# Kernel optimization log

Hardware: AMD Instinct MI355X
Metric: run time of the kernel (lower is better)

## Reference

```python
import jax, jax.numpy as jnp
import numpy as np

N_M, N_D, E, D, H, O = 50000, 20000, 600000, 128, 128, 64


def _graph_conv(x_src, x_dst, src, dst, W_rel, b_rel, W_root, ew=None):
    # PyG GraphConv: lin_rel(scatter_add(msg)) + lin_root(x_dst)
    msg = x_src[src]                       # [E, d_src] gather
    if ew is not None:
        msg = msg * ew[:, None]            # edge-weighted messages
    agg = jax.ops.segment_sum(msg, dst, num_segments=x_dst.shape[0])  # [N_dst, d_src]
    return agg @ W_rel + b_rel + x_dst @ W_root


def setup_inputs() -> dict:
    key = jax.random.key(0)
    ks = jax.random.split(key, 16)
    s = 1.0 / np.sqrt(D)
    inp = {
        "x_meas": jax.random.normal(ks[0], (N_M, D), jnp.float32),
        "x_dem": jax.random.normal(ks[1], (N_D, D), jnp.float32),
        "src_m": jax.random.randint(ks[2], (E,), 0, N_M, jnp.int32),
        "dst_m": jax.random.randint(ks[3], (E,), 0, N_M, jnp.int32),
        "src_b": jax.random.randint(ks[4], (E,), 0, N_M, jnp.int32),
        "dst_b": jax.random.randint(ks[5], (E,), 0, N_D, jnp.int32),
        "edge_weight": jax.random.normal(ks[6], (E,), jnp.float32),
        "W_rel1": jax.random.normal(ks[7], (D, H), jnp.float32) * s,
        "b_rel1": jnp.zeros((H,), jnp.float32),
        "W_root1": jax.random.normal(ks[8], (D, H), jnp.float32) * s,
        "W_rel2": jax.random.normal(ks[9], (D, H), jnp.float32) * s,
        "b_rel2": jnp.zeros((H,), jnp.float32),
        "W_root2": jax.random.normal(ks[10], (D, H), jnp.float32) * s,
        "W_rel3": jax.random.normal(ks[11], (H, H), jnp.float32) * s,
        "b_rel3": jnp.zeros((H,), jnp.float32),
        "W_root3": jax.random.normal(ks[12], (H, H), jnp.float32) * s,
        "W_lin": jax.random.normal(ks[13], (H, O), jnp.float32) * (1.0 / np.sqrt(H)),
        "b_lin": jnp.zeros((O,), jnp.float32),
    }
    return inp


def reference(x_meas, x_dem, src_m, dst_m, src_b, dst_b, edge_weight,
              W_rel1, b_rel1, W_root1, W_rel2, b_rel2, W_root2,
              W_rel3, b_rel3, W_root3, W_lin, b_lin):
    ew = jax.nn.sigmoid(edge_weight)
    movie_x = jax.nn.relu(_graph_conv(x_meas, x_meas, src_m, dst_m, W_rel1, b_rel1, W_root1))
    user_x = jax.nn.relu(_graph_conv(x_meas, x_dem, src_b, dst_b, W_rel2, b_rel2, W_root2, ew))
    user_x = jax.nn.relu(_graph_conv(movie_x, user_x, src_b, dst_b, W_rel3, b_rel3, W_root3, ew))
    return user_x @ W_lin + b_lin  # [N_D, O]
```

## Files before the change

kernel.cpp:

```cpp
#include <hip/hip_runtime.h>


typedef unsigned short u16;
typedef unsigned int u32;
typedef __attribute__((ext_vector_type(8))) short bf16x8;
typedef __attribute__((ext_vector_type(4))) float f32x4;

#define NMC 50000
#define NDC 20000
#define EC  600000
#define CM  128
#define CHM ((EC + CM - 1) / CM)
#define NWM8 (NMC / 4)
#define NWD8 (NDC / 4)

__device__ __forceinline__ float bf2f(u16 h) {
    union { u32 u; float f; } v; v.u = ((u32)h) << 16; return v.f;
}
__device__ __forceinline__ float uplo(u32 u) {
    union { u32 u; float f; } t; t.u = u << 16; return t.f;
}
__device__ __forceinline__ float uphi(u32 u) {
    union { u32 u; float f; } t; t.u = u & 0xffff0000u; return t.f;
}
__device__ __forceinline__ u16 f2bf(float f) {
    union { float f; u32 u; } v; v.f = f;
    u32 lsb = (v.u >> 16) & 1u;
    v.u += 0x7fffu + lsb;
    return (u16)(v.u >> 16);
}

__global__ __launch_bounds__(256)
void prep_hist(const int* __restrict__ dst_m, const int* __restrict__ dst_b,
               int* __restrict__ rank_m, int* __restrict__ rank_b,
               u32* __restrict__ histm, u32* __restrict__ histd,
               const float* __restrict__ xm, u16* __restrict__ xm_bf, int n8m,
               const float* __restrict__ xd, u16* __restrict__ xd_bf, int n8d,
               const float* __restrict__ w0, const float* __restrict__ w1,
               const float* __restrict__ w2, const float* __restrict__ w3,
               const float* __restrict__ w4, const float* __restrict__ w5,
               const float* __restrict__ w6, u16* __restrict__ wbuf,
               int TB, int TB2)
{
    __shared__ u32 h[NWM8];
    const int b = blockIdx.x;
    if (b < 2 * CM) {
        const bool isM = b < CM;
        const int nw = isM ? NWM8 : NWD8;
        for (int i = threadIdx.x; i < nw; i += 256) h[i] = 0;
        __syncthreads();
        if (isM) {
            const int e0 = b * CHM;
            const int e1 = min(EC, e0 + CHM);
            for (int e = e0 + threadIdx.x; e < e1; e += 256) {
                int d = dst_m[e];
                int sh = (d & 3) * 8;
                u32 old = atomicAdd(&h[d >> 2], 1u << sh);
                rank_m[e] = (old >> sh) & 0xffu;
            }
            __syncthreads();
            for (int i = threadIdx.x; i < nw; i += 256)
                histm[(size_t)b * NWM8 + i] = h[i];
        } else {
            const int bb = b - CM;
            const int e0 = bb * CHM;
            const int e1 = min(EC, e0 + CHM);
            for (int e = e0 + threadIdx.x; e < e1; e += 256) {
                int d = dst_b[e];
                int sh = (d & 3) * 8;
                u32 old = atomicAdd(&h[d >> 2], 1u << sh);
                rank_b[e] = (old >> sh) & 0xffu;
            }
            __syncthreads();
            for (int i = threadIdx.x; i < nw; i += 256)
                histd[(size_t)bb * NWD8 + i] = h[i];
        }
        return;
    }
    const int pb = b - 2 * CM;
    if (pb < TB + TB2) {
        const bool isM = pb < TB;
        const float* src = isM ? xm : xd;
        u16* dst = isM ? xm_bf : xd_bf;
        int n8 = isM ? n8m : n8d;
        int i = (pb - (isM ? 0 : TB)) * 256 + threadIdx.x;
        if (i >= n8) return;
        float4 a = ((const float4*)src)[2 * i];
        float4 c2 = ((const float4*)src)[2 * i + 1];
        ushort4 h0; h0.x = f2bf(a.x); h0.y = f2bf(a.y); h0.z = f2bf(a.z); h0.w = f2bf(a.w);
        ushort4 h1; h1.x = f2bf(c2.x); h1.y = f2bf(c2.y); h1.z = f2bf(c2.z); h1.w = f2bf(c2.w);
        ((ushort4*)dst)[2 * i]     = h0;
        ((ushort4*)dst)[2 * i + 1] = h1;
    } else {
        int bb = pb - TB - TB2;
        const int widx = bb >> 6;
        const int o    = ((bb & 63) << 8) + threadIdx.x;
        const int OC   = (widx == 6) ? 64 : 128;
        if (o >= OC * 128) return;
        const float* W;
        switch (widx) {
            case 0: W = w0; break; case 1: W = w1; break; case 2: W = w2; break;
            case 3: W = w3; break; case 4: W = w4; break; case 5: W = w5; break;
            default: W = w6;
        }
        int j = o & 7;
        int lane = (o >> 3) & 63;
        int n, c;
        if (OC == 128) { n = (o >> 9) & 7; c = o >> 12; }
        else           { n = (o >> 9) & 3; c = o >> 11; }
        int col = n * 16 + (lane & 15);
        int k   = c * 32 + (lane >> 4) * 8 + j;
        wbuf[widx * 16384 + o] = f2bf(W[k * OC + col]);
    }
}

__global__ __launch_bounds__(256)
void basescan8(u32* __restrict__ histm, u32* __restrict__ histd,
               int* __restrict__ deg_m, int* __restrict__ deg_b)
{
    int t = blockIdx.x * 256 + threadIdx.x;
    int idx = t >> 2;
    const int q = t & 3;
    u32* hist; int* deg; int NW;
    if (idx < NWM8)             { hist = histm; deg = deg_m; NW = NWM8; }
    else if (idx < NWM8 + NWD8) { hist = histd; deg = deg_b; NW = NWD8; idx -= NWM8; }
    else return;

    u32* hp = hist + (size_t)(q * 32) * NW + idx;
    u32 v[32];
#pragma unroll
    for (int j = 0; j < 32; ++j) v[j] = hp[(size_t)j * NW];
    u32 run = 0;
#pragma unroll
    for (int j = 0; j < 32; ++j) { u32 x = v[j]; v[j] = run; run += x; }
    u32 x = run;
    u32 y = __shfl_up(x, 1, 4); if (q >= 1) x += y;
    y = __shfl_up(x, 2, 4);     if (q >= 2) x += y;
    const u32 base = x - run;
#pragma unroll
    for (int j = 0; j < 32; ++j) hp[(size_t)j * NW] = base + v[j];
    if (q == 3) {
        deg[4 * idx + 0] = (int)(x & 0xffu);
        deg[4 * idx + 1] = (int)((x >> 8) & 0xffu);
        deg[4 * idx + 2] = (int)((x >> 16) & 0xffu);
        deg[4 * idx + 3] = (int)(x >> 24);
    }
}

__device__ __forceinline__ int wave_incl_scan(int v, int lane) {
#pragma unroll
    for (int off = 1; off < 64; off <<= 1) {
        int t = __shfl_up(v, off, 64);
        if (lane >= off) v += t;
    }
    return v;
}

__global__ __launch_bounds__(1024)
void scan2_kernel(const int* __restrict__ degA, int* __restrict__ rpA, int nA,
                  const int* __restrict__ degB, int* __restrict__ rpB, int nB)
{
    const int* deg = blockIdx.x ? degB : degA;
    int* rp = blockIdx.x ? rpB : rpA;
    int n = blockIdx.x ? nB : nA;

    __shared__ int wsum[16];
    __shared__ int carry;
    const int tid = threadIdx.x, lane = tid & 63, wid = tid >> 6;
    if (tid == 0) carry = 0;
    __syncthreads();

    for (int base = 0; base < n; base += 8192) {
        int idx = base + tid * 8;
        int4 va = make_int4(0, 0, 0, 0), vb = make_int4(0, 0, 0, 0);
        if (idx + 7 < n) {
            va = *(const int4*)(deg + idx);
            vb = *(const int4*)(deg + idx + 4);
        } else {
            if (idx + 0 < n) va.x = deg[idx + 0];
            if (idx + 1 < n) va.y = deg[idx + 1];
            if (idx + 2 < n) va.z = deg[idx + 2];
            if (idx + 3 < n) va.w = deg[idx + 3];
            if (idx + 4 < n) vb.x = deg[idx + 4];
            if (idx + 5 < n) vb.y = deg[idx + 5];
            if (idx + 6 < n) vb.z = deg[idx + 6];
            if (idx + 7 < n) vb.w = deg[idx + 7];
        }
        int sa = va.x + va.y + va.z + va.w;
        int s = sa + vb.x + vb.y + vb.z + vb.w;
        int incl = wave_incl_scan(s, lane);
        if (lane == 63) wsum[wid] = incl;
        __syncthreads();
        if (wid == 0) {
            int t = (lane < 16) ? wsum[lane] : 0;
            int ti = wave_incl_scan(t, lane);
            if (lane < 16) wsum[lane] = ti - t;
        }
        __syncthreads();
        int base_t = carry + wsum[wid] + incl - s;
        if (idx + 7 < n) {
            int4 st;
            st.x = base_t;
            st.y = base_t + va.x;
            st.z = base_t + va.x + va.y;
            st.w = base_t + va.x + va.y + va.z;
            *(int4*)(rp + idx) = st;
            int b4 = base_t + sa;
            st.x = b4;
            st.y = b4 + vb.x;
            st.z = b4 + vb.x + vb.y;
            st.w = b4 + vb.x + vb.y + vb.z;
            *(int4*)(rp + idx + 4) = st;
        } else {
            int r = base_t;
            if (idx + 0 < n) rp[idx + 0] = r; r += va.x;
            if (idx + 1 < n) rp[idx + 1] = r; r += va.y;
            if (idx + 2 < n) rp[idx + 2] = r; r += va.z;
            if (idx + 3 < n) rp[idx + 3] = r; r += va.w;
            if (idx + 4 < n) rp[idx + 4] = r; r += vb.x;
            if (idx + 5 < n) rp[idx + 5] = r; r += vb.y;
            if (idx + 6 < n) rp[idx + 6] = r; r += vb.z;
            if (idx + 7 < n) rp[idx + 7] = r;
        }
        __syncthreads();
        if (tid == 1023) carry += wsum[15] + incl;
        __syncthreads();
    }
    if (tid == 0) rp[n] = carry;
}

__global__ __launch_bounds__(256)
void fill_kernel(const int* __restrict__ src_m, const int* __restrict__ dst_m,
                 const int* __restrict__ src_b, const int* __restrict__ dst_b,
                 const float* __restrict__ edge_w,
                 const int* __restrict__ rp_m, const int* __restrict__ rp_b,
                 const int* __restrict__ rank_m, const int* __restrict__ rank_b,
                 const u32* __restrict__ histm, const u32* __restrict__ histd,
                 int* __restrict__ srcs_m, int2* __restrict__ edges_b, int E)
{
    int t = blockIdx.x * 256 + threadIdx.x;
    if (t < E) {
        int d = dst_m[t];
        int c = t / CHM;
        u32 pk = histm[(size_t)c * NWM8 + (d >> 2)];
        int base = (pk >> ((d & 3) * 8)) & 0xffu;
        int pos = rp_m[d] + base + rank_m[t];
        srcs_m[pos] = src_m[t];
    } else if (t < 2 * E) {
        int e = t - E;
        int d = dst_b[e];
        int c = e / CHM;
        u32 pkb = histd[(size_t)c * NWD8 + (d >> 2)];
        int base = (pkb >> ((d & 3) * 8)) & 0xffu;
        int pos = rp_b[d] + base + rank_b[e];
        float x = edge_w[e];
        int2 pk;
        pk.x = src_b[e];
        pk.y = __float_as_int(1.0f / (1.0f + __expf(-x)));
        edges_b[pos] = pk;
    }
}

__global__ __launch_bounds__(256)
void gather12(const u16* __restrict__ Xb,
              const int* __restrict__ srcs_m, const int2* __restrict__ edges_b,
              const int* __restrict__ rp_m, const int* __restrict__ rp_b,
              u16* __restrict__ agg1, u16* __restrict__ agg2, int NM, int ND)
{
    const int h  = blockIdx.x * 16 + (threadIdx.x >> 4);
    const int cl = threadIdx.x & 15;
    float a0 = 0.f, a1 = 0.f, a2 = 0.f, a3 = 0.f;
    float a4 = 0.f, a5 = 0.f, a6 = 0.f, a7 = 0.f;

    if (h < NM) {
        int i   = rp_m[h];
        int end = rp_m[h + 1];
        for (; i + 8 <= end; i += 8) {
            int s[8];
#pragma unroll
            for (int k = 0; k < 8; ++k) s[k] = srcs_m[i + k];
            uint4 v[8];
#pragma unroll
            for (int k = 0; k < 8; ++k)
                v[k] = *(const uint4*)(Xb + (size_t)s[k] * 128 + cl * 8);
#pragma unroll
            for (int k = 0; k < 8; ++k) {
                a0 += uplo(v[k].x); a1 += uphi(v[k].x);
                a2 += uplo(v[k].y); a3 += uphi(v[k].y);
                a4 += uplo(v[k].z); a5 += uphi(v[k].z);
                a6 += uplo(v[k].w); a7 += uphi(v[k].w);
            }
        }
        for (; i < end; ++i) {
            uint4 v = *(const uint4*)(Xb + (size_t)srcs_m[i] * 128 + cl * 8);
            a0 += uplo(v.x); a1 += uphi(v.x);
            a2 += uplo(v.y); a3 += uphi(v.y);
            a4 += uplo(v.z); a5 += uphi(v.z);
            a6 += uplo(v.w); a7 += uphi(v.w);
        }
        uint4 st;
        st.x = (u32)f2bf(a0) | ((u32)f2bf(a1) << 16);
        st.y = (u32)f2bf(a2) | ((u32)f2bf(a3) << 16);
        st.z = (u32)f2bf(a4) | ((u32)f2bf(a5) << 16);
        st.w = (u32)f2bf(a6) | ((u32)f2bf(a7) << 16);
        *(uint4*)(agg1 + (size_t)h * 128 + cl * 8) = st;
    } else if (h < NM + ND) {
        int node = h - NM;
        int i   = rp_b[node];
        int end = rp_b[node + 1];
        for (; i + 8 <= end; i += 8) {
            int2 p[8];
#pragma unroll
            for (int k = 0; k < 8; ++k) p[k] = edges_b[i + k];
            uint4 v[8];
#pragma unroll
            for (int k = 0; k < 8; ++k)
                v[k] = *(const uint4*)(Xb + (size_t)p[k].x * 128 + cl * 8);
#pragma unroll
            for (int k = 0; k < 8; ++k) {
                float w = __int_as_float(p[k].y);
                a0 = fmaf(w, uplo(v[k].x), a0); a1 = fmaf(w, uphi(v[k].x), a1);
                a2 = fmaf(w, uplo(v[k].y), a2); a3 = fmaf(w, uphi(v[k].y), a3);
                a4 = fmaf(w, uplo(v[k].z), a4); a5 = fmaf(w, uphi(v[k].z), a5);
                a6 = fmaf(w, uplo(v[k].w), a6); a7 = fmaf(w, uphi(v[k].w), a7);
            }
        }
        for (; i < end; ++i) {
            int2 pk = edges_b[i];
            float w = __int_as_float(pk.y);
            uint4 v = *(const uint4*)(Xb + (size_t)pk.x * 128 + cl * 8);
            a0 = fmaf(w, uplo(v.x), a0); a1 = fmaf(w, uphi(v.x), a1);
            a2 = fmaf(w, uplo(v.y), a2); a3 = fmaf(w, uphi(v.y), a3);
            a4 = fmaf(w, uplo(v.z), a4); a5 = fmaf(w, uphi(v.z), a5);
            a6 = fmaf(w, uplo(v.w), a6); a7 = fmaf(w, uphi(v.w), a7);
        }
        uint4 st;
        st.x = (u32)f2bf(a0) | ((u32)f2bf(a1) << 16);
        st.y = (u32)f2bf(a2) | ((u32)f2bf(a3) << 16);
        st.z = (u32)f2bf(a4) | ((u32)f2bf(a5) << 16);
        st.w = (u32)f2bf(a6) | ((u32)f2bf(a7) << 16);
        *(uint4*)(agg2 + (size_t)node * 128 + cl * 8) = st;
    }
}

__global__ __launch_bounds__(256)
void gather3_kernel(const u16* __restrict__ Mv, const int2* __restrict__ edges_b,
                    const int* __restrict__ rp_b, u16* __restrict__ agg3, int ND)
{
    const int node = blockIdx.x * 16 + (threadIdx.x >> 4);
    if (node >= ND) return;
    const int cl = threadIdx.x & 15;
    int i   = rp_b[node];
    int end = rp_b[node + 1];
    float a0 = 0.f, a1 = 0.f, a2 = 0.f, a3 = 0.f;
    float a4 = 0.f, a5 = 0.f, a6 = 0.f, a7 = 0.f;

    for (; i + 8 <= end; i += 8) {
        int2 p[8];
#pragma unroll
        for (int k = 0; k < 8; ++k) p[k] = edges_b[i + k];
        uint4 v[8];
#pragma unroll
        for (int k = 0; k < 8; ++k)
            v[k] = *(const uint4*)(Mv + (size_t)p[k].x * 128 + cl * 8);
#pragma unroll
        for (int k = 0; k < 8; ++k) {
            float w = __int_as_float(p[k].y);
            a0 = fmaf(w, uplo(v[k].x), a0); a1 = fmaf(w, uphi(v[k].x), a1);
            a2 = fmaf(w, uplo(v[k].y), a2); a3 = fmaf(w, uphi(v[k].y), a3);
            a4 = fmaf(w, uplo(v[k].z), a4); a5 = fmaf(w, uphi(v[k].z), a5);
            a6 = fmaf(w, uplo(v[k].w), a6); a7 = fmaf(w, uphi(v[k].w), a7);
        }
    }
    for (; i < end; ++i) {
        int2 pk = edges_b[i];
        float w = __int_as_float(pk.y);
        uint4 v = *(const uint4*)(Mv + (size_t)pk.x * 128 + cl * 8);
        a0 = fmaf(w, uplo(v.x), a0); a1 = fmaf(w, uphi(v.x), a1);
        a2 = fmaf(w, uplo(v.y), a2); a3 = fmaf(w, uphi(v.y), a3);
        a4 = fmaf(w, uplo(v.z), a4); a5 = fmaf(w, uphi(v.z), a5);
        a6 = fmaf(w, uplo(v.w), a6); a7 = fmaf(w, uphi(v.w), a7);
    }
    uint4 st;
    st.x = (u32)f2bf(a0) | ((u32)f2bf(a1) << 16);
    st.y = (u32)f2bf(a2) | ((u32)f2bf(a3) << 16);
    st.z = (u32)f2bf(a4) | ((u32)f2bf(a5) << 16);
    st.w = (u32)f2bf(a6) | ((u32)f2bf(a7) << 16);
    *(uint4*)(agg3 + (size_t)node * 128 + cl * 8) = st;
}

__global__ __launch_bounds__(256)
void conv12_mfma(const u16* __restrict__ agg1, const u16* __restrict__ w1r,
                 const float* __restrict__ b1, const u16* __restrict__ xm_bf,
                 const u16* __restrict__ w1o, u16* __restrict__ C1, int N1, int cb1,
                 const u16* __restrict__ agg2, const u16* __restrict__ w2r,
                 const float* __restrict__ b2, const u16* __restrict__ xd_bf,
                 const u16* __restrict__ w2o, u16* __restrict__ C2, int N2)
{
    __shared__ u16 sW[16384];

    const bool seg1 = (int)blockIdx.x < cb1;
    const u16 *A0, *A1p, *Wr, *Wo; const float* bias; u16* C; int N, base;
    if (seg1) { A0 = agg1; A1p = xm_bf; Wr = w1r; Wo = w1o; bias = b1; C = C1; N = N1; base = blockIdx.x; }
    else      { A0 = agg2; A1p = xd_bf; Wr = w2r; Wo = w2o; bias = b2; C = C2; N = N2; base = blockIdx.x - cb1; }

    const int tid  = threadIdx.x;
    const int lane = tid & 63;
    const int m0   = (base * 4 + (tid >> 6)) * 32;
    const int lr   = lane & 15;
    const int quad = lane >> 4;

    int r0 = m0 + lr;      if (r0 >= N) r0 = N - 1;
    int r1 = m0 + 16 + lr; if (r1 >= N) r1 = N - 1;

    f32x4 acc[2][8];
#pragma unroll
    for (int mt = 0; mt < 2; ++mt)
#pragma unroll
        for (int n = 0; n < 8; ++n) acc[mt][n] = (f32x4){0.f, 0.f, 0.f, 0.f};

    for (int i = tid; i < 2048; i += 256)
        ((uint4*)sW)[i] = ((const uint4*)Wr)[i];
    __syncthreads();
#pragma unroll
    for (int c = 0; c < 4; ++c) {
        const int kb = c * 32 + quad * 8;
        bf16x8 a0 = *(const bf16x8*)(A0 + (size_t)r0 * 128 + kb);
        bf16x8 a1 = *(const bf16x8*)(A0 + (size_t)r1 * 128 + kb);
        const u16* wp = sW + c * 4096 + lane * 8;
#pragma unroll
        for (int n = 0; n < 8; ++n) {
            bf16x8 b = *(const bf16x8*)(wp + n * 512);
            acc[0][n] = __builtin_amdgcn_mfma_f32_16x16x32_bf16(a0, b, acc[0][n], 0, 0, 0);
            acc[1][n] = __builtin_amdgcn_mfma_f32_16x16x32_bf16(a1, b, acc[1][n], 0, 0, 0);
        }
    }
    __syncthreads();

    for (int i = tid; i < 2048; i += 256)
        ((uint4*)sW)[i] = ((const uint4*)Wo)[i];
    __syncthreads();
#pragma unroll
    for (int c = 0; c < 4; ++c) {
        const int kb = c * 32 + quad * 8;
        bf16x8 a0 = *(const bf16x8*)(A1p + (size_t)r0 * 128 + kb);
        bf16x8 a1 = *(const bf16x8*)(A1p + (size_t)r1 * 128 + kb);
        const u16* wp = sW + c * 4096 + lane * 8;
#pragma unroll
        for (int n = 0; n < 8; ++n) {
            bf16x8 b = *(const bf16x8*)(wp + n * 512);
            acc[0][n] = __builtin_amdgcn_mfma_f32_16x16x32_bf16(a0, b, acc[0][n], 0, 0, 0);
            acc[1][n] = __builtin_amdgcn_mfma_f32_16x16x32_bf16(a1, b, acc[1][n], 0, 0, 0);
        }
    }

#pragma unroll
    for (int mt = 0; mt < 2; ++mt) {
#pragma unroll
        for (int n = 0; n < 8; ++n) {
            const int col = n * 16 + lr;
            const float b = bias[col];
#pragma unroll
            for (int r = 0; r < 4; ++r) {
                int row = m0 + mt * 16 + quad * 4 + r;
                if (row >= N) continue;
                C[(size_t)row * 128 + col] = f2bf(fmaxf(acc[mt][n][r] + b, 0.f));
            }
        }
    }
}

__global__ __launch_bounds__(256)
void conv3_lin(const u16* __restrict__ A1, const u16* __restrict__ Wr,
               const float* __restrict__ bias3,
               const u16* __restrict__ A2, const u16* __restrict__ Wo,
               const u16* __restrict__ Wl, const float* __restrict__ bias_l,
               float* __restrict__ out, int N)
{
    __shared__ u16 lds[17408 + 8192];
    u16* tile = lds;
    u16* sWl  = lds + 17408;

    const int tid  = threadIdx.x;
    const int lane = tid & 63;
    const int wv   = tid >> 6;
    const int wbase = wv * 32;
    const int m0   = (blockIdx.x * 4 + wv) * 32;
    const int lr   = lane & 15;
    const int quad = lane >> 4;

    int r0 = m0 + lr;      if (r0 >= N) r0 = N - 1;
    int r1 = m0 + 16 + lr; if (r1 >= N) r1 = N - 1;

    f32x4 acc[2][8];
#pragma unroll
    for (int mt = 0; mt < 2; ++mt)
#pragma unroll
        for (int n = 0; n < 8; ++n) acc[mt][n] = (f32x4){0.f, 0.f, 0.f, 0.f};

    for (int i = tid; i < 1024; i += 256)
        ((uint4*)sWl)[i] = ((const uint4*)Wl)[i];
    for (int i = tid; i < 2048; i += 256)
        ((uint4*)lds)[i] = ((const uint4*)Wr)[i];
    __syncthreads();
#pragma unroll
    for (int c = 0; c < 4; ++c) {
        const int kb = c * 32 + quad * 8;
        bf16x8 a0 = *(const bf16x8*)(A1 + (size_t)r0 * 128 + kb);
        bf16x8 a1 = *(const bf16x8*)(A1 + (size_t)r1 * 128 + kb);
        const u16* wp = lds + c * 4096 + lane * 8;
#pragma unroll
        for (int n = 0; n < 8; ++n) {
            bf16x8 b = *(const bf16x8*)(wp + n * 512);
            acc[0][n] = __builtin_amdgcn_mfma_f32_16x16x32_bf16(a0, b, acc[0][n], 0, 0, 0);
            acc[1][n] = __builtin_amdgcn_mfma_f32_16x16x32_bf16(a1, b, acc[1][n], 0, 0, 0);
        }
    }
    __syncthreads();
    for (int i = tid; i < 2048; i += 256)
        ((uint4*)lds)[i] = ((const uint4*)Wo)[i];
    __syncthreads();
// ... 36 lines not shown
#pragma unroll
    for (int c = 0; c < 4; ++c) {
        const int kb = c * 32 + quad * 8;
        bf16x8 a0 = *(const bf16x8*)(tile + (wbase + lr) * 136 + kb);
        bf16x8 a1 = *(const bf16x8*)(tile + (wbase + 16 + lr) * 136 + kb);
#pragma unroll
        for (int n = 0; n < 4; ++n) {
            bf16x8 b = *(const bf16x8*)(sWl + c * 2048 + n * 512 + lane * 8);
            acc2[0][n] = __builtin_amdgcn_mfma_f32_16x16x32_bf16(a0, b, acc2[0][n], 0, 0, 0);
            acc2[1][n] = __builtin_amdgcn_mfma_f32_16x16x32_bf16(a1, b, acc2[1][n], 0, 0, 0);
        }
    }

#pragma unroll
    for (int mt = 0; mt < 2; ++mt) {
#pragma unroll
        for (int n = 0; n < 4; ++n) {
            const int col = n * 16 + lr;
            const float b = bias_l[col];
#pragma unroll
            for (int r = 0; r < 4; ++r) {
                int row = m0 + mt * 16 + quad * 4 + r;
                if (row >= N) continue;
                out[(size_t)row * 64 + col] = acc2[mt][n][r] + b;
            }
        }
    }
}

extern "C" void kernel_launch(void* const* d_in, const int* in_sizes, int n_in,
                              void* d_out, int out_size, void* d_ws, size_t ws_size,
                              hipStream_t stream)
{
    const float* x_meas  = (const float*)d_in[0];
    const float* x_dem   = (const float*)d_in[1];
    const int*   src_m   = (const int*)d_in[2];
    const int*   dst_m   = (const int*)d_in[3];
    const int*   src_b   = (const int*)d_in[4];
    const int*   dst_b   = (const int*)d_in[5];
    const float* edge_w  = (const float*)d_in[6];
    const float* W_rel1  = (const float*)d_in[7];
    const float* b_rel1  = (const float*)d_in[8];
    const float* W_root1 = (const float*)d_in[9];
    const float* W_rel2  = (const float*)d_in[10];
    const float* b_rel2  = (const float*)d_in[11];
    const float* W_root2 = (const float*)d_in[12];
    const float* W_rel3  = (const float*)d_in[13];
    const float* b_rel3  = (const float*)d_in[14];
    const float* W_root3 = (const float*)d_in[15];
    const float* W_lin   = (const float*)d_in[16];
    const float* b_lin   = (const float*)d_in[17];
    float* out = (float*)d_out;

    const int NM = NMC, ND = NDC, E = EC;

    char* p = (char*)d_ws;
    auto alloc = [&](size_t bytes) { char* r = p; p += (bytes + 511) & ~(size_t)511; return r; };
    u32*   histm   = (u32*)alloc((size_t)CM * NWM8 * 4);
    u32*   histd   = (u32*)alloc((size_t)CM * NWD8 * 4);
    int*   deg_m   = (int*)alloc((size_t)NM * 4);
    int*   deg_b   = (int*)alloc((size_t)ND * 4);
    int*   rp_m    = (int*)alloc((size_t)(NM + 1) * 4);
    int*   rp_b    = (int*)alloc((size_t)(ND + 1) * 4);
    int*   srcs_m  = (int*)alloc((size_t)E * 4);
    int2*  edges_b = (int2*)alloc((size_t)E * 8);
    u16*   agg1    = (u16*)alloc((size_t)NM * 128 * 2);
    u16*   agg2    = (u16*)alloc((size_t)ND * 128 * 2);
    u16*   movie   = (u16*)alloc((size_t)NM * 128 * 2);
    u16*   t2      = (u16*)alloc((size_t)ND * 128 * 2);
    u16*   xd_bf   = (u16*)alloc((size_t)ND * 128 * 2);
    u16*   wbuf    = (u16*)alloc(7 * 16384 * 2);
    int* rank_m = (int*)agg1;
    int* rank_b = rank_m + E;
    u16* xm_bf  = movie;
    u16* agg3   = agg1;

    const int TB  = (NM * 16 + 255) / 256;
    const int TB2 = (ND * 16 + 255) / 256;
    const int WB  = 448;
    const int HB  = (2 * E + 255) / 256;

    prep_hist<<<2 * CM + TB + TB2 + WB, 256, 0, stream>>>(
        dst_m, dst_b, rank_m, rank_b, histm, histd,
        x_meas, xm_bf, NM * 16, x_dem, xd_bf, ND * 16,
        W_rel1, W_root1, W_rel2, W_root2, W_rel3, W_root3, W_lin, wbuf,
        TB, TB2);

    basescan8<<<((NWM8 + NWD8) * 4 + 255) / 256, 256, 0, stream>>>(histm, histd, deg_m, deg_b);
    scan2_kernel<<<2, 1024, 0, stream>>>(deg_m, rp_m, NM, deg_b, rp_b, ND);
    fill_kernel<<<HB, 256, 0, stream>>>(src_m, dst_m, src_b, dst_b, edge_w,
                                        rp_m, rp_b, rank_m, rank_b,
                                        histm, histd, srcs_m, edges_b, E);

    gather12<<<(NM + ND + 15) / 16, 256, 0, stream>>>(xm_bf, srcs_m, edges_b,
                                                      rp_m, rp_b, agg1, agg2, NM, ND);

    const int cb1 = (NM + 127) / 128;
    const int cb2 = (ND + 127) / 128;
    u16* w1r = wbuf + 0 * 16384; u16* w1o = wbuf + 1 * 16384;
    u16* w2r = wbuf + 2 * 16384; u16* w2o = wbuf + 3 * 16384;
    u16* w3r = wbuf + 4 * 16384; u16* w3o = wbuf + 5 * 16384;
    u16* wl  = wbuf + 6 * 16384;
    conv12_mfma<<<cb1 + cb2, 256, 0, stream>>>(agg1, w1r, b_rel1, xm_bf, w1o, movie, NM, cb1,
                                               agg2, w2r, b_rel2, xd_bf, w2o, t2,    ND);

    gather3_kernel<<<(ND + 15) / 16, 256, 0, stream>>>(movie, edges_b, rp_b, agg3, ND);

    conv3_lin<<<cb2, 256, 0, stream>>>(agg3, w3r, b_rel3, t2, w3o, wl, b_lin, out, ND);
}
```

Baseline: 269.9 us.

## Fuse scan, fill, gather and conv stages into one flag-synchronized persistent kernel

Replaces the separate basescan, scan, fill, gather, conv12 and gather3 launches with a single kernel. Block ranges act as stages and wait on global atomic counters set by earlier stages, which removes several kernel launch boundaries and lets later stages start as soon as their inputs are posted. The device-wide scan is also reworked to use 256 threads with 32 elements each. xm_bf gets its own buffer instead of aliasing movie, and the flags are zeroed by an extra prep_hist block. This depends on blocks being dispatched in index order to avoid deadlock, and it adds spin-wait overhead, including a whole-grid barrier before the gather stage.

```diff
diff --git a/kernel.cpp b/kernel.cpp
--- a/kernel.cpp
+++ b/kernel.cpp
@@ -14,6 +14,22 @@
 #define NWM8 (NMC / 4)
 #define NWD8 (NDC / 4)
 
+#define B_P0 274
+#define O1 274
+#define O2 276
+#define O3 4964
+#define O4 9339
+#define O5 9887
+#define PEND 11137
+#define CB1 391
+#define CB2 157
+
+#define F_BASE 0
+#define F_SCAN 1
+#define F_FILL 2
+#define F_CONV1 3
+#define F_CFLAG 8
+
 __device__ __forceinline__ float bf2f(u16 h) {
     union { u32 u; float f; } v; v.u = ((u32)h) << 16; return v.f;
 }
@@ -28,6 +44,34 @@
     u32 lsb = (v.u >> 16) & 1u;
     v.u += 0x7fffu + lsb;
     return (u16)(v.u >> 16);
+}
+
+__device__ __forceinline__ void wait_flag(int* flag, int thresh) {
+    if (threadIdx.x == 0) {
+        int it = 0;
+        while (__hip_atomic_load(flag, __ATOMIC_RELAXED, __HIP_MEMORY_SCOPE_AGENT) < thresh) {
+            __builtin_amdgcn_s_sleep(2);
+            if (++it > 100000000) break;
+        }
+        __builtin_amdgcn_fence(__ATOMIC_ACQUIRE, "agent");
+    }
+    __syncthreads();
+}
+__device__ __forceinline__ void post_flag(int* flag, int inc) {
+    __syncthreads();
+    if (threadIdx.x == 0) {
+        __builtin_amdgcn_fence(__ATOMIC_RELEASE, "agent");
+        __hip_atomic_fetch_add(flag, inc, __ATOMIC_RELAXED, __HIP_MEMORY_SCOPE_AGENT);
+    }
+}
+
+__device__ __forceinline__ int wave_incl_scan(int v, int lane) {
+#pragma unroll
+    for (int off = 1; off < 64; off <<= 1) {
+        int t = __shfl_up(v, off, 64);
+        if (lane >= off) v += t;
+    }
+    return v;
 }
 
 __global__ __launch_bounds__(256)
@@ -40,7 +84,7 @@
                const float* __restrict__ w2, const float* __restrict__ w3,
                const float* __restrict__ w4, const float* __restrict__ w5,
                const float* __restrict__ w6, u16* __restrict__ wbuf,
-               int TB, int TB2)
+               int* __restrict__ flags, int TB, int TB2)
 {
     __shared__ u32 h[NWM8];
     const int b = blockIdx.x;
@@ -93,6 +137,10 @@
         ((ushort4*)dst)[2 * i + 1] = h1;
     } else {
         int bb = pb - TB - TB2;
+        if (bb >= 448) {
+            for (int i = threadIdx.x; i < 1024; i += 256) flags[i] = 0;
+            return;
+        }
         const int widx = bb >> 6;
         const int o    = ((bb & 63) << 8) + threadIdx.x;
         const int OC   = (widx == 6) ? 64 : 128;
@@ -115,199 +163,277 @@
 }
 
 __global__ __launch_bounds__(256)
-void basescan8(u32* __restrict__ histm, u32* __restrict__ histd,
-               int* __restrict__ deg_m, int* __restrict__ deg_b)
+void pipeline(u32* __restrict__ histm, u32* __restrict__ histd,
+              int* __restrict__ deg_m, int* __restrict__ deg_b,
+              int* __restrict__ rp_m, int* __restrict__ rp_b,
+              const int* __restrict__ src_m, const int* __restrict__ dst_m,
+              const int* __restrict__ src_b, const int* __restrict__ dst_b,
+              const float* __restrict__ edge_w,
+              const int* __restrict__ rank_m, const int* __restrict__ rank_b,
+              int* __restrict__ srcs_m, int2* __restrict__ edges_b,
+              const u16* __restrict__ xm_bf, const u16* __restrict__ xd_bf,
+              u16* __restrict__ agg1, u16* __restrict__ agg2,
+              const u16* __restrict__ wbuf,
+              const float* __restrict__ b1, const float* __restrict__ b2,
+              u16* __restrict__ movie, u16* __restrict__ t2,
+              u16* __restrict__ agg3, int* __restrict__ flags)
 {
-    int t = blockIdx.x * 256 + threadIdx.x;
-    int idx = t >> 2;
-    const int q = t & 3;
-    u32* hist; int* deg; int NW;
-    if (idx < NWM8)             { hist = histm; deg = deg_m; NW = NWM8; }
-    else if (idx < NWM8 + NWD8) { hist = histd; deg = deg_b; NW = NWD8; idx -= NWM8; }
-    else return;
-
-    u32* hp = hist + (size_t)(q * 32) * NW + idx;
-    u32 v[32];
-#pragma unroll
-    for (int j = 0; j < 32; ++j) v[j] = hp[(size_t)j * NW];
-    u32 run = 0;
-#pragma unroll
-    for (int j = 0; j < 32; ++j) { u32 x = v[j]; v[j] = run; run += x; }
-    u32 x = run;
-    u32 y = __shfl_up(x, 1, 4); if (q >= 1) x += y;
-    y = __shfl_up(x, 2, 4);     if (q >= 2) x += y;
-    const u32 base = x - run;
-#pragma unroll
-    for (int j = 0; j < 32; ++j) hp[(size_t)j * NW] = base + v[j];
-    if (q == 3) {
-        deg[4 * idx + 0] = (int)(x & 0xffu);
-        deg[4 * idx + 1] = (int)((x >> 8) & 0xffu);
-        deg[4 * idx + 2] = (int)((x >> 16) & 0xffu);
-        deg[4 * idx + 3] = (int)(x >> 24);
-    }
-}
-
-__device__ __forceinline__ int wave_incl_scan(int v, int lane) {
-#pragma unroll
-    for (int off = 1; off < 64; off <<= 1) {
-        int t = __shfl_up(v, off, 64);
-        if (lane >= off) v += t;
-    }
-    return v;
-}
-
-__global__ __launch_bounds__(1024)
-void scan2_kernel(const int* __restrict__ degA, int* __restrict__ rpA, int nA,
-                  const int* __restrict__ degB, int* __restrict__ rpB, int nB)
-{
-    const int* deg = blockIdx.x ? degB : degA;
-    int* rp = blockIdx.x ? rpB : rpA;
-    int n = blockIdx.x ? nB : nA;
-
-    __shared__ int wsum[16];
-    __shared__ int carry;
-    const int tid = threadIdx.x, lane = tid & 63, wid = tid >> 6;
-    if (tid == 0) carry = 0;
-    __syncthreads();
-
-    for (int base = 0; base < n; base += 8192) {
-        int idx = base + tid * 8;
-        int4 va = make_int4(0, 0, 0, 0), vb = make_int4(0, 0, 0, 0);
-        if (idx + 7 < n) {
-            va = *(const int4*)(deg + idx);
-            vb = *(const int4*)(deg + idx + 4);
+    const int b   = blockIdx.x;
+    const int tid = threadIdx.x;
+
+    if (b < B_P0) {
+        int t = b * 256 + tid;
+        int idx = t >> 2;
+        const int q = t & 3;
+        u32* hist; int* deg; int NW;
+        bool act = true;
+        if (idx < NWM8)             { hist = histm; deg = deg_m; NW = NWM8; }
+        else if (idx < NWM8 + NWD8) { hist = histd; deg = deg_b; NW = NWD8; idx -= NWM8; }
+        else act = false;
+        if (act) {
+            u32* hp = hist + (size_t)(q * 32) * NW + idx;
+            u32 v[32];
+#pragma unroll
+            for (int j = 0; j < 32; ++j) v[j] = hp[(size_t)j * NW];
+            u32 run = 0;
+#pragma unroll
+            for (int j = 0; j < 32; ++j) { u32 x = v[j]; v[j] = run; run += x; }
+            u32 x = run;
+            u32 y = __shfl_up(x, 1, 4); if (q >= 1) x += y;
+            y = __shfl_up(x, 2, 4);     if (q >= 2) x += y;
+            const u32 base = x - run;
+#pragma unroll
+            for (int j = 0; j < 32; ++j) hp[(size_t)j * NW] = base + v[j];
+            if (q == 3) {
+                deg[4 * idx + 0] = (int)(x & 0xffu);
+                deg[4 * idx + 1] = (int)((x >> 8) & 0xffu);
+                deg[4 * idx + 2] = (int)((x >> 16) & 0xffu);
+                deg[4 * idx + 3] = (int)(x >> 24);
+            }
+        }
+        post_flag(&flags[F_BASE], 1);
+    } else if (b < O2) {
+        wait_flag(&flags[F_BASE], B_P0);
+        const bool isM = (b == O1);
+        const int* deg = isM ? deg_m : deg_b;
+        int* rp = isM ? rp_m : rp_b;
+        const int n = isM ? NMC : NDC;
+        __shared__ int ws4[4], wx4[4];
+        __shared__ int carryS;
+        if (tid == 0) carryS = 0;
+        __syncthreads();
+        const int lane = tid & 63, wid = tid >> 6;
+        for (int base = 0; base < n; base += 8192) {
+            int idx = base + tid * 32;
+            int v[32];
+#pragma unroll
+            for (int k = 0; k < 8; ++k) {
+                int4 qv = make_int4(0, 0, 0, 0);
+                int i4 = idx + 4 * k;
+                if (i4 + 3 < n) qv = *(const int4*)(deg + i4);
+                else {
+                    if (i4 + 0 < n) qv.x = deg[i4 + 0];
+                    if (i4 + 1 < n) qv.y = deg[i4 + 1];
+                    if (i4 + 2 < n) qv.z = deg[i4 + 2];
+                    if (i4 + 3 < n) qv.w = deg[i4 + 3];
+                }
+                v[4 * k] = qv.x; v[4 * k + 1] = qv.y; v[4 * k + 2] = qv.z; v[4 * k + 3] = qv.w;
+            }
+            int s = 0;
+#pragma unroll
+            for (int k = 0; k < 32; ++k) s += v[k];
+            int incl = wave_incl_scan(s, lane);
+            if (lane == 63) ws4[wid] = incl;
+            __syncthreads();
+            if (tid == 0) { int r = 0; for (int j = 0; j < 4; ++j) { wx4[j] = r; r += ws4[j]; } }
+            __syncthreads();
+            int c0 = carryS;
+            int r = c0 + wx4[wid] + incl - s;
+#pragma unroll
+            for (int k = 0; k < 32; ++k) { if (idx + k < n) rp[idx + k] = r; r += v[k]; }
+            __syncthreads();
+            if (tid == 0) carryS = c0 + wx4[3] + ws4[3];
+            __syncthreads();
+        }
+        if (tid == 0) rp[n] = carryS;
+        post_flag(&flags[F_SCAN], 1);
+    } else if (b < O3) {
+        wait_flag(&flags[F_SCAN], 2);
+        int t = (b - O2) * 256 + tid;
+        if (t < EC) {
+            int d = dst_m[t];
+            int c = t / CHM;
+            u32 pk = histm[(size_t)c * NWM8 + (d >> 2)];
+            int base = (pk >> ((d & 3) * 8)) & 0xffu;
+            int pos = rp_m[d] + base + rank_m[t];
+            srcs_m[pos] = src_m[t];
+        } else if (t < 2 * EC) {
+            int e = t - EC;
+            int d = dst_b[e];
+            int c = e / CHM;
+            u32 pkb = histd[(size_t)c * NWD8 + (d >> 2)];
+            int base = (pkb >> ((d & 3) * 8)) & 0xffu;
+            int pos = rp_b[d] + base + rank_b[e];
+            float x = edge_w[e];
+            int2 pk;
+            pk.x = src_b[e];
+            pk.y = __float_as_int(1.0f / (1.0f + __expf(-x)));
+            edges_b[pos] = pk;
+        }
+        post_flag(&flags[F_FILL], 1);
+    } else if (b < O4) {
+        wait_flag(&flags[F_FILL], 4688);
+        const int g  = b - O3;
+        const int h  = g * 16 + (tid >> 4);
+        const int cl = tid & 15;
+        float a0 = 0.f, a1 = 0.f, a2 = 0.f, a3 = 0.f;
+        float a4 = 0.f, a5 = 0.f, a6 = 0.f, a7 = 0.f;
+        if (h < NMC) {
+            int i = rp_m[h], end = rp_m[h + 1];
+            for (; i + 8 <= end; i += 8) {
+                int s[8];
+#pragma unroll
+                for (int k = 0; k < 8; ++k) s[k] = srcs_m[i + k];
+                uint4 v[8];
+#pragma unroll
+                for (int k = 0; k < 8; ++k)
+                    v[k] = *(const uint4*)(xm_bf + (size_t)s[k] * 128 + cl * 8);
+#pragma unroll
+                for (int k = 0; k < 8; ++k) {
+                    a0 += uplo(v[k].x); a1 += uphi(v[k].x);
+                    a2 += uplo(v[k].y); a3 += uphi(v[k].y);
+                    a4 += uplo(v[k].z); a5 += uphi(v[k].z);
+                    a6 += uplo(v[k].w); a7 += uphi(v[k].w);
+                }
+            }
+            for (; i < end; ++i) {
+                uint4 v = *(const uint4*)(xm_bf + (size_t)srcs_m[i] * 128 + cl * 8);
+                a0 += uplo(v.x); a1 += uphi(v.x);
+                a2 += uplo(v.y); a3 += uphi(v.y);
+                a4 += uplo(v.z); a5 += uphi(v.z);
+                a6 += uplo(v.w); a7 += uphi(v.w);
+            }
+            uint4 st;
+            st.x = (u32)f2bf(a0) | ((u32)f2bf(a1) << 16);
+            st.y = (u32)f2bf(a2) | ((u32)f2bf(a3) << 16);
+            st.z = (u32)f2bf(a4) | ((u32)f2bf(a5) << 16);
+            st.w = (u32)f2bf(a6) | ((u32)f2bf(a7) << 16);
+            *(uint4*)(agg1 + (size_t)h * 128 + cl * 8) = st;
         } else {
-            if (idx + 0 < n) va.x = deg[idx + 0];
-            if (idx + 1 < n) va.y = deg[idx + 1];
-            if (idx + 2 < n) va.z = deg[idx + 2];
-            if (idx + 3 < n) va.w = deg[idx + 3];
-            if (idx + 4 < n) vb.x = deg[idx + 4];
-            if (idx + 5 < n) vb.y = deg[idx + 5];
-            if (idx + 6 < n) vb.z = deg[idx + 6];
-            if (idx + 7 < n) vb.w = deg[idx + 7];
-        }
-        int sa = va.x + va.y + va.z + va.w;
-        int s = sa + vb.x + vb.y + vb.z + vb.w;
-        int incl = wave_incl_scan(s, lane);
-        if (lane == 63) wsum[wid] = incl;
-        __syncthreads();
-        if (wid == 0) {
-            int t = (lane < 16) ? wsum[lane] : 0;
-            int ti = wave_incl_scan(t, lane);
-            if (lane < 16) wsum[lane] = ti - t;
-        }
-        __syncthreads();
-        int base_t = carry + wsum[wid] + incl - s;
-        if (idx + 7 < n) {
-            int4 st;
-            st.x = base_t;
-            st.y = base_t + va.x;
-            st.z = base_t + va.x + va.y;
-            st.w = base_t + va.x + va.y + va.z;
-            *(int4*)(rp + idx) = st;
-            int b4 = base_t + sa;
-            st.x = b4;
-            st.y = b4 + vb.x;
-            st.z = b4 + vb.x + vb.y;
-            st.w = b4 + vb.x + vb.y + vb.z;
-            *(int4*)(rp + idx + 4) = st;
-        } else {
-            int r = base_t;
-            if (idx + 0 < n) rp[idx + 0] = r; r += va.x;
-            if (idx + 1 < n) rp[idx + 1] = r; r += va.y;
-            if (idx + 2 < n) rp[idx + 2] = r; r += va.z;
-            if (idx + 3 < n) rp[idx + 3] = r; r += va.w;
-            if (idx + 4 < n) rp[idx + 4] = r; r += vb.x;
-            if (idx + 5 < n) rp[idx + 5] = r; r += vb.y;
-            if (idx + 6 < n) rp[idx + 6] = r; r += vb.z;
-            if (idx + 7 < n) rp[idx + 7] = r;
-        }
-        __syncthreads();
-        if (tid == 1023) carry += wsum[15] + incl;
-        __syncthreads();
-    }
-    if (tid == 0) rp[n] = carry;
-}
-
-__global__ __launch_bounds__(256)
-void fill_kernel(const int* __restrict__ src_m, const int* __restrict__ dst_m,
-                 const int* __restrict__ src_b, const int* __restrict__ dst_b,
-                 const float* __restrict__ edge_w,
-                 const int* __restrict__ rp_m, const int* __restrict__ rp_b,
-                 const int* __restrict__ rank_m, const int* __restrict__ rank_b,
-                 const u32* __restrict__ histm, const u32* __restrict__ histd,
-                 int* __restrict__ srcs_m, int2* __restrict__ edges_b, int E)
-{
-    int t = blockIdx.x * 256 + threadIdx.x;
-    if (t < E) {
-        int d = dst_m[t];
-        int c = t / CHM;
-        u32 pk = histm[(size_t)c * NWM8 + (d >> 2)];
-        int base = (pk >> ((d & 3) * 8)) & 0xffu;
-        int pos = rp_m[d] + base + rank_m[t];
-        srcs_m[pos] = src_m[t];
-    } else if (t < 2 * E) {
-        int e = t - E;
-        int d = dst_b[e];
-        int c = e / CHM;
-        u32 pkb = histd[(size_t)c * NWD8 + (d >> 2)];
-        int base = (pkb >> ((d & 3) * 8)) & 0xffu;
-        int pos = rp_b[d] + base + rank_b[e];
-        float x = edge_w[e];
-        int2 pk;
-        pk.x = src_b[e];
-        pk.y = __float_as_int(1.0f / (1.0f + __expf(-x)));
-        edges_b[pos] = pk;
-    }
-}
-
-__global__ __launch_bounds__(256)
-void gather12(const u16* __restrict__ Xb,
-              const int* __restrict__ srcs_m, const int2* __restrict__ edges_b,
-              const int* __restrict__ rp_m, const int* __restrict__ rp_b,
-              u16* __restrict__ agg1, u16* __restrict__ agg2, int NM, int ND)
-{
-    const int h  = blockIdx.x * 16 + (threadIdx.x >> 4);
-    const int cl = threadIdx.x & 15;
-    float a0 = 0.f, a1 = 0.f, a2 = 0.f, a3 = 0.f;
-    float a4 = 0.f, a5 = 0.f, a6 = 0.f, a7 = 0.f;
-
-    if (h < NM) {
-        int i   = rp_m[h];
-        int end = rp_m[h + 1];
-        for (; i + 8 <= end; i += 8) {
-            int s[8];
-#pragma unroll
-            for (int k = 0; k < 8; ++k) s[k] = srcs_m[i + k];
-            uint4 v[8];
-#pragma unroll
-            for (int k = 0; k < 8; ++k)
-                v[k] = *(const uint4*)(Xb + (size_t)s[k] * 128 + cl * 8);
-#pragma unroll
-            for (int k = 0; k < 8; ++k) {
-                a0 += uplo(v[k].x); a1 += uphi(v[k].x);
-                a2 += uplo(v[k].y); a3 += uphi(v[k].y);
-                a4 += uplo(v[k].z); a5 += uphi(v[k].z);
-                a6 += uplo(v[k].w); a7 += uphi(v[k].w);
-            }
-        }
-        for (; i < end; ++i) {
-            uint4 v = *(const uint4*)(Xb + (size_t)srcs_m[i] * 128 + cl * 8);
-            a0 += uplo(v.x); a1 += uphi(v.x);
-            a2 += uplo(v.y); a3 += uphi(v.y);
-            a4 += uplo(v.z); a5 += uphi(v.z);
-            a6 += uplo(v.w); a7 += uphi(v.w);
-        }
-        uint4 st;
-        st.x = (u32)f2bf(a0) | ((u32)f2bf(a1) << 16);
-        st.y = (u32)f2bf(a2) | ((u32)f2bf(a3) << 16);
-        st.z = (u32)f2bf(a4) | ((u32)f2bf(a5) << 16);
-        st.w = (u32)f2bf(a6) | ((u32)f2bf(a7) << 16);
-        *(uint4*)(agg1 + (size_t)h * 128 + cl * 8) = st;
-    } else if (h < NM + ND) {
-        int node = h - NM;
-        int i   = rp_b[node];
-        int end = rp_b[node + 1];
+            int node = h - NMC;
+            int i = rp_b[node], end = rp_b[node + 1];
+            for (; i + 8 <= end; i += 8) {
+                int2 p[8];
+#pragma unroll
+                for (int k = 0; k < 8; ++k) p[k] = edges_b[i + k];
+                uint4 v[8];
+#pragma unroll
+                for (int k = 0; k < 8; ++k)
+                    v[k] = *(const uint4*)(xm_bf + (size_t)p[k].x * 128 + cl * 8);
+#pragma unroll
+                for (int k = 0; k < 8; ++k) {
+                    float w = __int_as_float(p[k].y);
+                    a0 = fmaf(w, uplo(v[k].x), a0); a1 = fmaf(w, uphi(v[k].x), a1);
+                    a2 = fmaf(w, uplo(v[k].y), a2); a3 = fmaf(w, uphi(v[k].y), a3);
+                    a4 = fmaf(w, uplo(v[k].z), a4); a5 = fmaf(w, uphi(v[k].z), a5);
+                    a6 = fmaf(w, uplo(v[k].w), a6); a7 = fmaf(w, uphi(v[k].w), a7);
+                }
+            }
+            for (; i < end; ++i) {
+                int2 pk = edges_b[i];
+                float w = __int_as_float(pk.y);
+                uint4 v = *(const uint4*)(xm_bf + (size_t)pk.x * 128 + cl * 8);
+                a0 = fmaf(w, uplo(v.x), a0); a1 = fmaf(w, uphi(v.x), a1);
+                a2 = fmaf(w, uplo(v.y), a2); a3 = fmaf(w, uphi(v.y), a3);
+                a4 = fmaf(w, uplo(v.z), a4); a5 = fmaf(w, uphi(v.z), a5);
+                a6 = fmaf(w, uplo(v.w), a6); a7 = fmaf(w, uphi(v.w), a7);
+            }
+            uint4 st;
+            st.x = (u32)f2bf(a0) | ((u32)f2bf(a1) << 16);
+            st.y = (u32)f2bf(a2) | ((u32)f2bf(a3) << 16);
+            st.z = (u32)f2bf(a4) | ((u32)f2bf(a5) << 16);
+            st.w = (u32)f2bf(a6) | ((u32)f2bf(a7) << 16);
+            *(uint4*)(agg2 + (size_t)node * 128 + cl * 8) = st;
+        }
+        const int cidx = (g < 3125) ? (g >> 3) : (CB1 + ((g - 3125) >> 3));
+        post_flag(&flags[F_CFLAG + cidx], 1);
+    } else if (b < O5) {
+        const int b4 = b - O4;
+        const bool seg1 = b4 < CB1;
+        const int base = seg1 ? b4 : (b4 - CB1);
+        const int thr = seg1 ? min(8, 3125 - 8 * base) : min(8, 1250 - 8 * base);
+        wait_flag(&flags[F_CFLAG + (seg1 ? base : CB1 + base)], thr);
+
+        const u16* A0 = seg1 ? agg1 : agg2;
+        const u16* Ar = seg1 ? xm_bf : xd_bf;
+        const u16* Wr = wbuf + (seg1 ? 0 : 2) * 16384;
+        const u16* Wo = wbuf + (seg1 ? 1 : 3) * 16384;
+        const float* bias = seg1 ? b1 : b2;
+        u16* C = seg1 ? movie : t2;
+        const int N = seg1 ? NMC : NDC;
+
+        const int lane = tid & 63;
+        const int m0   = (base * 4 + (tid >> 6)) * 32;
+        const int lr   = lane & 15;
+        const int quad = lane >> 4;
+        int r0 = m0 + lr;      if (r0 >= N) r0 = N - 1;
+        int r1 = m0 + 16 + lr; if (r1 >= N) r1 = N - 1;
+
+        f32x4 acc[2][8];
+#pragma unroll
+        for (int mt = 0; mt < 2; ++mt)
+#pragma unroll
+            for (int n = 0; n < 8; ++n) acc[mt][n] = (f32x4){0.f, 0.f, 0.f, 0.f};
+
+#pragma unroll
+        for (int c = 0; c < 4; ++c) {
+            const int kb = c * 32 + quad * 8;
+            bf16x8 a0v = *(const bf16x8*)(A0 + (size_t)r0 * 128 + kb);
+            bf16x8 a1v = *(const bf16x8*)(A0 + (size_t)r1 * 128 + kb);
+            const u16* wp = Wr + c * 4096 + lane * 8;
+#pragma unroll
+            for (int n = 0; n < 8; ++n) {
+                bf16x8 bv = *(const bf16x8*)(wp + n * 512);
+                acc[0][n] = __builtin_amdgcn_mfma_f32_16x16x32_bf16(a0v, bv, acc[0][n], 0, 0, 0);
+                acc[1][n] = __builtin_amdgcn_mfma_f32_16x16x32_bf16(a1v, bv, acc[1][n], 0, 0, 0);
+            }
+        }
+#pragma unroll
+        for (int c = 0; c < 4; ++c) {
+            const int kb = c * 32 + quad * 8;
+            bf16x8 a0v = *(const bf16x8*)(Ar + (size_t)r0 * 128 + kb);
+            bf16x8 a1v = *(const bf16x8*)(Ar + (size_t)r1 * 128 + kb);
+            const u16* wp = Wo + c * 4096 + lane * 8;
+#pragma unroll
+            for (int n = 0; n < 8; ++n) {
+                bf16x8 bv = *(const bf16x8*)(wp + n * 512);
+                acc[0][n] = __builtin_amdgcn_mfma_f32_16x16x32_bf16(a0v, bv, acc[0][n], 0, 0, 0);
+                acc[1][n] = __builtin_amdgcn_mfma_f32_16x16x32_bf16(a1v, bv, acc[1][n], 0, 0, 0);
+            }
+        }
+#pragma unroll
+        for (int mt = 0; mt < 2; ++mt) {
+#pragma unroll
+            for (int n = 0; n < 8; ++n) {
+                const int col = n * 16 + lr;
+                const float bb = bias[col];
+#pragma unroll
+                for (int r = 0; r < 4; ++r) {
+                    int row = m0 + mt * 16 + quad * 4 + r;
+                    if (row >= N) continue;
+                    C[(size_t)row * 128 + col] = f2bf(fmaxf(acc[mt][n][r] + bb, 0.f));
+                }
+            }
+        }
+        if (seg1) post_flag(&flags[F_CONV1], 1);
+    } else {
+        wait_flag(&flags[F_CONV1], CB1);
+        const int g = b - O5;
+        const int node = g * 16 + (tid >> 4);
+        const int cl = tid & 15;
+        int i = rp_b[node], end = rp_b[node + 1];
+        float a0 = 0.f, a1 = 0.f, a2 = 0.f, a3 = 0.f;
+        float a4 = 0.f, a5 = 0.f, a6 = 0.f, a7 = 0.f;
         for (; i + 8 <= end; i += 8) {
             int2 p[8];
 #pragma unroll
@@ -315,7 +441,7 @@
             uint4 v[8];
 #pragma unroll
             for (int k = 0; k < 8; ++k)
-                v[k] = *(const uint4*)(Xb + (size_t)p[k].x * 128 + cl * 8);
+                v[k] = *(const uint4*)(movie + (size_t)p[k].x * 128 + cl * 8);
 #pragma unroll
             for (int k = 0; k < 8; ++k) {
                 float w = __int_as_float(p[k].y);
@@ -328,7 +454,7 @@
         for (; i < end; ++i) {
             int2 pk = edges_b[i];
             float w = __int_as_float(pk.y);
-            uint4 v = *(const uint4*)(Xb + (size_t)pk.x * 128 + cl * 8);
+            uint4 v = *(const uint4*)(movie + (size_t)pk.x * 128 + cl * 8);
             a0 = fmaf(w, uplo(v.x), a0); a1 = fmaf(w, uphi(v.x), a1);
             a2 = fmaf(w, uplo(v.y), a2); a3 = fmaf(w, uphi(v.y), a3);
             a4 = fmaf(w, uplo(v.z), a4); a5 = fmaf(w, uphi(v.z), a5);
@@ -339,134 +465,7 @@
         st.y = (u32)f2bf(a2) | ((u32)f2bf(a3) << 16);
         st.z = (u32)f2bf(a4) | ((u32)f2bf(a5) << 16);
         st.w = (u32)f2bf(a6) | ((u32)f2bf(a7) << 16);
-        *(uint4*)(agg2 + (size_t)node * 128 + cl * 8) = st;
-    }
-}
-
-__global__ __launch_bounds__(256)
-void gather3_kernel(const u16* __restrict__ Mv, const int2* __restrict__ edges_b,
-                    const int* __restrict__ rp_b, u16* __restrict__ agg3, int ND)
-{
-    const int node = blockIdx.x * 16 + (threadIdx.x >> 4);
-    if (node >= ND) return;
-    const int cl = threadIdx.x & 15;
-    int i   = rp_b[node];
-    int end = rp_b[node + 1];
-    float a0 = 0.f, a1 = 0.f, a2 = 0.f, a3 = 0.f;
-    float a4 = 0.f, a5 = 0.f, a6 = 0.f, a7 = 0.f;
-
-    for (; i + 8 <= end; i += 8) {
-        int2 p[8];
-#pragma unroll
-        for (int k = 0; k < 8; ++k) p[k] = edges_b[i + k];
-        uint4 v[8];
-#pragma unroll
-        for (int k = 0; k < 8; ++k)
-            v[k] = *(const uint4*)(Mv + (size_t)p[k].x * 128 + cl * 8);
-#pragma unroll
-        for (int k = 0; k < 8; ++k) {
-            float w = __int_as_float(p[k].y);
-            a0 = fmaf(w, uplo(v[k].x), a0); a1 = fmaf(w, uphi(v[k].x), a1);
-            a2 = fmaf(w, uplo(v[k].y), a2); a3 = fmaf(w, uphi(v[k].y), a3);
-            a4 = fmaf(w, uplo(v[k].z), a4); a5 = fmaf(w, uphi(v[k].z), a5);
-            a6 = fmaf(w, uplo(v[k].w), a6); a7 = fmaf(w, uphi(v[k].w), a7);
-        }
-    }
-    for (; i < end; ++i) {
-        int2 pk = edges_b[i];
-        float w = __int_as_float(pk.y);
-        uint4 v = *(const uint4*)(Mv + (size_t)pk.x * 128 + cl * 8);
-        a0 = fmaf(w, uplo(v.x), a0); a1 = fmaf(w, uphi(v.x), a1);
-        a2 = fmaf(w, uplo(v.y), a2); a3 = fmaf(w, uphi(v.y), a3);
-        a4 = fmaf(w, uplo(v.z), a4); a5 = fmaf(w, uphi(v.z), a5);
-        a6 = fmaf(w, uplo(v.w), a6); a7 = fmaf(w, uphi(v.w), a7);
-    }
-    uint4 st;
-    st.x = (u32)f2bf(a0) | ((u32)f2bf(a1) << 16);
-    st.y = (u32)f2bf(a2) | ((u32)f2bf(a3) << 16);
-    st.z = (u32)f2bf(a4) | ((u32)f2bf(a5) << 16);
-    st.w = (u32)f2bf(a6) | ((u32)f2bf(a7) << 16);
-    *(uint4*)(agg3 + (size_t)node * 128 + cl * 8) = st;
-}
-
-__global__ __launch_bounds__(256)
-void conv12_mfma(const u16* __restrict__ agg1, const u16* __restrict__ w1r,
-                 const float* __restrict__ b1, const u16* __restrict__ xm_bf,
-                 const u16* __restrict__ w1o, u16* __restrict__ C1, int N1, int cb1,
-                 const u16* __restrict__ agg2, const u16* __restrict__ w2r,
-                 const float* __restrict__ b2, const u16* __restrict__ xd_bf,
-                 const u16* __restrict__ w2o, u16* __restrict__ C2, int N2)
-{
-    __shared__ u16 sW[16384];
-
-    const bool seg1 = (int)blockIdx.x < cb1;
-    const u16 *A0, *A1p, *Wr, *Wo; const float* bias; u16* C; int N, base;
-    if (seg1) { A0 = agg1; A1p = xm_bf; Wr = w1r; Wo = w1o; bias = b1; C = C1; N = N1; base = blockIdx.x; }
-    else      { A0 = agg2; A1p = xd_bf; Wr = w2r; Wo = w2o; bias = b2; C = C2; N = N2; base = blockIdx.x - cb1; }
-
-    const int tid  = threadIdx.x;
-    const int lane = tid & 63;
-    const int m0   = (base * 4 + (tid >> 6)) * 32;
-    const int lr   = lane & 15;
-    const int quad = lane >> 4;
-
-    int r0 = m0 + lr;      if (r0 >= N) r0 = N - 1;
-    int r1 = m0 + 16 + lr; if (r1 >= N) r1 = N - 1;
-
-    f32x4 acc[2][8];
-#pragma unroll
-    for (int mt = 0; mt < 2; ++mt)
-#pragma unroll
-        for (int n = 0; n < 8; ++n) acc[mt][n] = (f32x4){0.f, 0.f, 0.f, 0.f};
-
-    for (int i = tid; i < 2048; i += 256)
-        ((uint4*)sW)[i] = ((const uint4*)Wr)[i];
-    __syncthreads();
-#pragma unroll
-    for (int c = 0; c < 4; ++c) {
-        const int kb = c * 32 + quad * 8;
-        bf16x8 a0 = *(const bf16x8*)(A0 + (size_t)r0 * 128 + kb);
-        bf16x8 a1 = *(const bf16x8*)(A0 + (size_t)r1 * 128 + kb);
-        const u16* wp = sW + c * 4096 + lane * 8;
-#pragma unroll
-        for (int n = 0; n < 8; ++n) {
-            bf16x8 b = *(const bf16x8*)(wp + n * 512);
-            acc[0][n] = __builtin_amdgcn_mfma_f32_16x16x32_bf16(a0, b, acc[0][n], 0, 0, 0);
-            acc[1][n] = __builtin_amdgcn_mfma_f32_16x16x32_bf16(a1, b, acc[1][n], 0, 0, 0);
-        }
-    }
-    __syncthreads();
-
-    for (int i = tid; i < 2048; i += 256)
-        ((uint4*)sW)[i] = ((const uint4*)Wo)[i];
-    __syncthreads();
-#pragma unroll
-    for (int c = 0; c < 4; ++c) {
-        const int kb = c * 32 + quad * 8;
-        bf16x8 a0 = *(const bf16x8*)(A1p + (size_t)r0 * 128 + kb);
-        bf16x8 a1 = *(const bf16x8*)(A1p + (size_t)r1 * 128 + kb);
-        const u16* wp = sW + c * 4096 + lane * 8;
-#pragma unroll
-        for (int n = 0; n < 8; ++n) {
-            bf16x8 b = *(const bf16x8*)(wp + n * 512);
-            acc[0][n] = __builtin_amdgcn_mfma_f32_16x16x32_bf16(a0, b, acc[0][n], 0, 0, 0);
-            acc[1][n] = __builtin_amdgcn_mfma_f32_16x16x32_bf16(a1, b, acc[1][n], 0, 0, 0);
-        }
-    }
-
-#pragma unroll
-    for (int mt = 0; mt < 2; ++mt) {
-#pragma unroll
-        for (int n = 0; n < 8; ++n) {
-            const int col = n * 16 + lr;
-            const float b = bias[col];
-#pragma unroll
-            for (int r = 0; r < 4; ++r) {
-                int row = m0 + mt * 16 + quad * 4 + r;
-                if (row >= N) continue;
-                C[(size_t)row * 128 + col] = f2bf(fmaxf(acc[mt][n][r] + b, 0.f));
-            }
-        }
+        *(uint4*)(agg3 + (size_t)node * 128 + cl * 8) = st;
     }
 }
 
@@ -609,7 +608,7 @@
     const float* b_lin   = (const float*)d_in[17];
     float* out = (float*)d_out;
 
-    const int NM = NMC, ND = NDC, E = EC;
+    const int NM = NMC, ND = NDC;
 
     char* p = (char*)d_ws;
     auto alloc = [&](size_t bytes) { char* r = p; p += (bytes + 511) & ~(size_t)511; return r; };
@@ -619,49 +618,37 @@
     int*   deg_b   = (int*)alloc((size_t)ND * 4);
     int*   rp_m    = (int*)alloc((size_t)(NM + 1) * 4);
     int*   rp_b    = (int*)alloc((size_t)(ND + 1) * 4);
-    int*   srcs_m  = (int*)alloc((size_t)E * 4);
-    int2*  edges_b = (int2*)alloc((size_t)E * 8);
+    int*   srcs_m  = (int*)alloc((size_t)EC * 4);
+    int2*  edges_b = (int2*)alloc((size_t)EC * 8);
+    u16*   xm_bf   = (u16*)alloc((size_t)NM * 128 * 2);
+    u16*   movie   = (u16*)alloc((size_t)NM * 128 * 2);
     u16*   agg1    = (u16*)alloc((size_t)NM * 128 * 2);
     u16*   agg2    = (u16*)alloc((size_t)ND * 128 * 2);
-    u16*   movie   = (u16*)alloc((size_t)NM * 128 * 2);
+    u16*   xd_bf   = (u16*)alloc((size_t)ND * 128 * 2);
     u16*   t2      = (u16*)alloc((size_t)ND * 128 * 2);
-    u16*   xd_bf   = (u16*)alloc((size_t)ND * 128 * 2);
     u16*   wbuf    = (u16*)alloc(7 * 16384 * 2);
+    int*   flags   = (int*)alloc(1024 * 4);
     int* rank_m = (int*)agg1;
-    int* rank_b = rank_m + E;
-    u16* xm_bf  = movie;
+    int* rank_b = rank_m + EC;
     u16* agg3   = agg1;
 
     const int TB  = (NM * 16 + 255) / 256;
     const int TB2 = (ND * 16 + 255) / 256;
     const int WB  = 448;
-    const int HB  = (2 * E + 255) / 256;
-
-    prep_hist<<<2 * CM + TB + TB2 + WB, 256, 0, stream>>>(
+
+    prep_hist<<<2 * CM + TB + TB2 + WB + 1, 256, 0, stream>>>(
         dst_m, dst_b, rank_m, rank_b, histm, histd,
         x_meas, xm_bf, NM * 16, x_dem, xd_bf, ND * 16,
         W_rel1, W_root1, W_rel2, W_root2, W_rel3, W_root3, W_lin, wbuf,
-        TB, TB2);
-
-    basescan8<<<((NWM8 + NWD8) * 4 + 255) / 256, 256, 0, stream>>>(histm, histd, deg_m, deg_b);
-    scan2_kernel<<<2, 1024, 0, stream>>>(deg_m, rp_m, NM, deg_b, rp_b, ND);
-    fill_kernel<<<HB, 256, 0, stream>>>(src_m, dst_m, src_b, dst_b, edge_w,
-                                        rp_m, rp_b, rank_m, rank_b,
-                                        histm, histd, srcs_m, edges_b, E);
-
-    gather12<<<(NM + ND + 15) / 16, 256, 0, stream>>>(xm_bf, srcs_m, edges_b,
-                                                      rp_m, rp_b, agg1, agg2, NM, ND);
-
-    const int cb1 = (NM + 127) / 128;
-    const int cb2 = (ND + 127) / 128;
-    u16* w1r = wbuf + 0 * 16384; u16* w1o = wbuf + 1 * 16384;
-    u16* w2r = wbuf + 2 * 16384; u16* w2o = wbuf + 3 * 16384;
+        flags, TB, TB2);
+
+    pipeline<<<PEND, 256, 0, stream>>>(
+        histm, histd, deg_m, deg_b, rp_m, rp_b,
+        src_m, dst_m, src_b, dst_b, edge_w, rank_m, rank_b,
+        srcs_m, edges_b, xm_bf, xd_bf, agg1, agg2, wbuf,
+        b_rel1, b_rel2, movie, t2, agg3, flags);
+
     u16* w3r = wbuf + 4 * 16384; u16* w3o = wbuf + 5 * 16384;
     u16* wl  = wbuf + 6 * 16384;
-    conv12_mfma<<<cb1 + cb2, 256, 0, stream>>>(agg1, w1r, b_rel1, xm_bf, w1o, movie, NM, cb1,
-                                               agg2, w2r, b_rel2, xd_bf, w2o, t2,    ND);
-
-    gather3_kernel<<<(ND + 15) / 16, 256, 0, stream>>>(movie, edges_b, rp_b, agg3, ND);
-
-    conv3_lin<<<cb2, 256, 0, stream>>>(agg3, w3r, b_rel3, t2, w3o, wl, b_lin, out, ND);
-}
+    conv3_lin<<<CB2, 256, 0, stream>>>(agg3, w3r, b_rel3, t2, w3o, wl, b_lin, out, ND);
+}
```

New measurement: 851.0 us. 215% more time.
